# Kernel optimization log

Measured on AMD Instinct MI355X. Metric: run time of the kernel, lower is better.

## Reference

```python
import jax, jax.numpy as jnp
import numpy as np

N_NODES = 100000
N_EDGES = 800000
C = 64        # in_channels == out_channels
H = 4         # num_heads
LN_EPS = 1e-5
SM_EPS = 1e-8


def setup_inputs() -> dict:
    key = jax.random.key(0)
    ks = jax.random.split(key, 8)
    return {
        "x": jax.random.normal(ks[0], (N_NODES, C), dtype=jnp.float32),
        "edge_index": jax.random.randint(ks[1], (2, N_EDGES), 0, N_NODES, dtype=jnp.int64),
        "edge_time": jax.random.uniform(ks[2], (N_EDGES,), dtype=jnp.float32),
        "current_time": 1,
        "W_w": jax.random.normal(ks[3], (C, C), dtype=jnp.float32) * (1.0 / np.sqrt(C)),
        "W_b": jnp.zeros((C,), dtype=jnp.float32),
        "attn_w": jax.random.normal(ks[4], (2 * C, H), dtype=jnp.float32) * (1.0 / np.sqrt(2 * C)),
        "attn_b": jnp.zeros((H,), dtype=jnp.float32),
        "decay_rate": jnp.full((1,), 0.1, dtype=jnp.float32),
        "proj_w": jax.random.normal(ks[5], (C * H, C), dtype=jnp.float32) * (1.0 / np.sqrt(C * H)),
        "proj_b": jnp.zeros((C,), dtype=jnp.float32),
        "ln_g": jnp.ones((C,), dtype=jnp.float32),
        "ln_b": jnp.zeros((C,), dtype=jnp.float32),
    }


def reference(x, edge_index, edge_time, current_time, W_w, W_b, attn_w, attn_b,
              decay_rate, proj_w, proj_b, ln_g, ln_b):
    num_nodes = x.shape[0]
    src, dst = edge_index[0], edge_index[1]

    # relation-specific transform (same Linear applied to src and dst node sets)
    h = x @ W_w + W_b                       # (N, C)
    h_src = h[src]                          # (E, C) gather
    h_dst = h[dst]                          # (E, C) gather

    # attention: Linear(2C -> H) + LeakyReLU(0.2)
    logits = h_src @ attn_w[:C] + h_dst @ attn_w[C:] + attn_b   # (E, H)
    scores = jax.nn.leaky_relu(logits, negative_slope=0.2)

    # temporal decay: exp(-softplus(lambda) * delta_t), multiplied pre-softmax
    delta_t = jnp.float32(current_time) - edge_time             # (E,)
    lam = jax.nn.softplus(decay_rate[0])
    scores = scores * jnp.exp(-lam * delta_t)[:, None]

    # segmented (per-destination) softmax over incoming edges
    smax = jax.ops.segment_max(scores, dst, num_segments=num_nodes)   # (N, H)
    e = jnp.exp(scores - smax[dst])                                   # (E, H)
    ssum = jax.ops.segment_sum(e, dst, num_segments=num_nodes)        # (N, H)
    attn = e / (ssum[dst] + SM_EPS)                                   # (E, H)

    # per-edge messages (E, C, H) -> (E, C*H), scatter-add to destinations
    msg = (h_src[:, :, None] * attn[:, None, :]).reshape(-1, C * H)
    agg = jax.ops.segment_sum(msg, dst, num_segments=num_nodes)       # (N, C*H)

    # single edge type -> mean over 1 message is identity
    out = agg @ proj_w + proj_b                                       # (N, C)
    # dropout p=0 (eval) -> identity; residual + LayerNorm + ReLU
    z = out + x
    mu = jnp.mean(z, axis=-1, keepdims=True)
    var = jnp.mean(jnp.square(z - mu), axis=-1, keepdims=True)
    y = ln_g * (z - mu) * jax.lax.rsqrt(var + LN_EPS) + ln_b
    return jax.nn.relu(y)
```

## Files before the change

kernel.cpp:

```cpp
#include <hip/hip_runtime.h>


typedef __attribute__((ext_vector_type(8))) short bf16x8;
typedef __attribute__((ext_vector_type(4))) float f32x4;

__device__ __forceinline__ unsigned short f2bf(float f) {
  unsigned int u = __float_as_uint(f);
  u += 0x7FFFu + ((u >> 16) & 1u);
  return (unsigned short)(u >> 16);
}
__device__ __forceinline__ float bf2f(unsigned short s) {
  return __uint_as_float(((unsigned int)s) << 16);
}
__device__ __forceinline__ unsigned int pk(float a, float b) {
  return (unsigned int)f2bf(a) | ((unsigned int)f2bf(b) << 16);
}
__device__ __forceinline__ float bflo(int u) {
  return __uint_as_float(((unsigned int)u) << 16);
}
__device__ __forceinline__ float bfhi(int u) {
  return __uint_as_float(((unsigned int)u) & 0xFFFF0000u);
}

__device__ __forceinline__ void split8(float4 a, float4 b, bf16x8* hi, bf16x8* lo) {
  float f[8] = {a.x, a.y, a.z, a.w, b.x, b.y, b.z, b.w};
  bf16x8 h, l;
  #pragma unroll
  for (int j = 0; j < 8; ++j) {
    unsigned short hs = f2bf(f[j]);
    h[j] = (short)hs;
    l[j] = (short)f2bf(f[j] - bf2f(hs));
  }
  *hi = h; *lo = l;
}

__global__ __launch_bounds__(256) void k_init(const float* __restrict__ Pw,
    const float* __restrict__ Ww, const float* __restrict__ Wb,
    const float* __restrict__ aw, unsigned short* __restrict__ Bf,
    unsigned short* __restrict__ Ah, unsigned short* __restrict__ Al,
    float* __restrict__ bc, int* __restrict__ deg, int N, int NBn)
{
  if ((int)blockIdx.x == NBn) {
    int t = threadIdx.x;
    for (int i = t; i < 5120; i += 256) {
      int j = i & 7, lane = (i >> 3) & 63, ks = (i >> 9) & 1, rb = i >> 10;
      int row = rb * 16 + (lane & 15);
      int k   = ks * 32 + (lane >> 4) * 8 + j;
      float w = 0.f;
      if (row < 64) {
        w = Ww[(size_t)k * 64 + row];
      } else if (row < 72) {
        int jj = row - 64;
        const float* ac = (jj < 4) ? (aw + jj) : (aw + 256 + (jj - 4));
        float s = 0.f;
        for (int c = 0; c < 64; ++c) s = fmaf(Ww[(size_t)k * 64 + c], ac[c * 4], s);
        w = s;
      }
      unsigned short hh = f2bf(w);
      Ah[i] = hh;
      Al[i] = f2bf(w - bf2f(hh));
    }
    if (t < 80) {
      float b = 0.f;
      if (t < 64) {
        b = Wb[t];
      } else if (t < 72) {
        int jj = t - 64;
        const float* ac = (jj < 4) ? (aw + jj) : (aw + 256 + (jj - 4));
        float s = 0.f;
        for (int c = 0; c < 64; ++c) s = fmaf(Wb[c], ac[c * 4], s);
        b = s;
      }
      bc[t] = b;
    }
    return;
  }
  int i = blockIdx.x * 256 + threadIdx.x;
  if (i < N) deg[i] = 0;
  if (i < 16384) {
    int j    = i & 7;
    int lane = (i >> 3) & 63;
    int cb   = (i >> 9) & 3;
    int ks   = i >> 11;
    int k    = ks * 32 + (lane >> 4) * 8 + j;
    int colg = cb * 16 + (lane & 15);
    Bf[i] = f2bf(Pw[(size_t)k * 64 + colg]);
  }
}

#define RBSTEP(ACC, RB) { \
  bf16x8 fh0 = *(const bf16x8*)(Ah + ((RB * 2 + 0) * 64 + lane) * 8); \
  bf16x8 fl0 = *(const bf16x8*)(Al + ((RB * 2 + 0) * 64 + lane) * 8); \
  bf16x8 fh1 = *(const bf16x8*)(Ah + ((RB * 2 + 1) * 64 + lane) * 8); \
  bf16x8 fl1 = *(const bf16x8*)(Al + ((RB * 2 + 1) * 64 + lane) * 8); \
  ACC = __builtin_amdgcn_mfma_f32_16x16x32_bf16(fh0, bh0, ACC, 0, 0, 0); \
  ACC = __builtin_amdgcn_mfma_f32_16x16x32_bf16(fl0, bh0, ACC, 0, 0, 0); \
  ACC = __builtin_amdgcn_mfma_f32_16x16x32_bf16(fh0, bl0, ACC, 0, 0, 0); \
  ACC = __builtin_amdgcn_mfma_f32_16x16x32_bf16(fh1, bh1, ACC, 0, 0, 0); \
  ACC = __builtin_amdgcn_mfma_f32_16x16x32_bf16(fl1, bh1, ACC, 0, 0, 0); \
  ACC = __builtin_amdgcn_mfma_f32_16x16x32_bf16(fh1, bl1, ACC, 0, 0, 0); \
}

__global__ __launch_bounds__(256, 4) void k_hd(const float* __restrict__ x,
    const unsigned short* __restrict__ Ah, const unsigned short* __restrict__ Al,
    const float* __restrict__ bc, const int* __restrict__ ei,
    unsigned short* __restrict__ h16, float4* __restrict__ u,
    float4* __restrict__ v, int* __restrict__ deg, int* __restrict__ rank,
    int N, int E, int NBe)
{
  if ((int)blockIdx.x < NBe) {
    int e0 = blockIdx.x * 1024 + threadIdx.x * 4;
    if (e0 + 3 < E) {
      int4 d4 = *(const int4*)(ei + E + e0);
      int4 r4;
      r4.x = atomicAdd(&deg[d4.x], 1);
      r4.y = atomicAdd(&deg[d4.y], 1);
      r4.z = atomicAdd(&deg[d4.z], 1);
      r4.w = atomicAdd(&deg[d4.w], 1);
      *(int4*)(rank + e0) = r4;
    } else {
      for (int e = e0; e < E; ++e) rank[e] = atomicAdd(&deg[ei[E + e]], 1);
    }
    return;
  }
  const int lane = threadIdx.x & 63;
  const int wv   = threadIdx.x >> 6;
  const int col  = lane & 15;
  const int quad = lane >> 4;

  const float4 bc0 = *(const float4*)(bc +  0 + quad * 4);
  const float4 bc1 = *(const float4*)(bc + 16 + quad * 4);
  const float4 bc2 = *(const float4*)(bc + 32 + quad * 4);
  const float4 bc3 = *(const float4*)(bc + 48 + quad * 4);
  const float4 bc4 = *(const float4*)(bc + 64 + quad * 4);

  const int base0 = (blockIdx.x - NBe) * 256 + wv * 64;
  for (int st = 0; st < 4; ++st) {
    const int node = base0 + st * 16 + col;
    const bool val = (node < N);
    const int nc = val ? node : N - 1;
    const float* xr = x + (size_t)nc * 64 + quad * 8;
    float4 x0 = *(const float4*)(xr);
    float4 x1 = *(const float4*)(xr + 4);
    float4 x2 = *(const float4*)(xr + 32);
    float4 x3 = *(const float4*)(xr + 36);
    bf16x8 bh0, bl0, bh1, bl1;
    split8(x0, x1, &bh0, &bl0);
    split8(x2, x3, &bh1, &bl1);

    f32x4 a0 = {0.f, 0.f, 0.f, 0.f};
    f32x4 a1 = {0.f, 0.f, 0.f, 0.f};
    f32x4 a2 = {0.f, 0.f, 0.f, 0.f};
    f32x4 a3 = {0.f, 0.f, 0.f, 0.f};
    f32x4 a4 = {0.f, 0.f, 0.f, 0.f};
    RBSTEP(a0, 0);
    RBSTEP(a1, 1);
    RBSTEP(a2, 2);
    RBSTEP(a3, 3);
    RBSTEP(a4, 4);

    if (val) {
      unsigned short* hr = h16 + (size_t)node * 64 + quad * 4;
      uint2 w0, w1, w2, w3;
      w0.x = pk(a0[0] + bc0.x, a0[1] + bc0.y);
      w0.y = pk(a0[2] + bc0.z, a0[3] + bc0.w);
      w1.x = pk(a1[0] + bc1.x, a1[1] + bc1.y);
      w1.y = pk(a1[2] + bc1.z, a1[3] + bc1.w);
      w2.x = pk(a2[0] + bc2.x, a2[1] + bc2.y);
      w2.y = pk(a2[2] + bc2.z, a2[3] + bc2.w);
      w3.x = pk(a3[0] + bc3.x, a3[1] + bc3.y);
      w3.y = pk(a3[2] + bc3.z, a3[3] + bc3.w);
      *(uint2*)(hr)      = w0;
      *(uint2*)(hr + 16) = w1;
      *(uint2*)(hr + 32) = w2;
      *(uint2*)(hr + 48) = w3;
      if (quad == 0)
        u[node] = make_float4(a4[0] + bc4.x, a4[1] + bc4.y, a4[2] + bc4.z, a4[3] + bc4.w);
      else if (quad == 1)
        v[node] = make_float4(a4[0] + bc4.x, a4[1] + bc4.y, a4[2] + bc4.z, a4[3] + bc4.w);
    }
  }
}

__global__ __launch_bounds__(256) void scan1(const int* __restrict__ deg,
    int* __restrict__ offs, int* __restrict__ bsums, int N)
{
  int i = blockIdx.x * 256 + threadIdx.x;
  int lane = threadIdx.x & 63;
  int w = threadIdx.x >> 6;
  int v = (i < N) ? deg[i] : 0;
  int s = v;
  #pragma unroll
  for (int d = 1; d < 64; d <<= 1) {
    int t = __shfl_up(s, d, 64);
    if (lane >= d) s += t;
  }
  __shared__ int wsum[4];
  if (lane == 63) wsum[w] = s;
  __syncthreads();
  int add = 0;
  if (w > 0) add += wsum[0];
  if (w > 1) add += wsum[1];
  if (w > 2) add += wsum[2];
  if (i < N) offs[i] = s - v + add;
  if (threadIdx.x == 255) bsums[blockIdx.x] = wsum[0] + wsum[1] + wsum[2] + wsum[3];
}

__global__ __launch_bounds__(512) void scan2(int* bsums, int NB)
{
  __shared__ int lds[512];
  int t = threadIdx.x;
  int v = (t < NB) ? bsums[t] : 0;
  lds[t] = v;
  __syncthreads();
  for (int s = 1; s < 512; s <<= 1) {
    int a = (t >= s) ? lds[t - s] : 0;
    __syncthreads();
    lds[t] += a;
    __syncthreads();
  }
  if (t < NB) bsums[t] = lds[t] - v;
}

__global__ __launch_bounds__(256) void k_fill(const int* __restrict__ ei,
    const float* __restrict__ et, const int* __restrict__ ctime,
    const float* __restrict__ drate, const float4* __restrict__ u,
    const float4* __restrict__ v, const float* __restrict__ attn_b,
    const int* __restrict__ offs, const int* __restrict__ bsums,
    const int* __restrict__ rank, int4* __restrict__ csr, int E)
{
  int e = blockIdx.x * 256 + threadIdx.x;
  if (e >= E) return;
  const int s = ei[e];
  const int d = ei[E + e];
  const float4 us = u[s];
  const float4 vd = v[d];
  const float4 ab = *(const float4*)attn_b;
  const float lam = log1pf(__expf(drate[0]));
  const float w = __expf(-lam * ((float)ctime[0] - et[e]));

  float4 o; float t;
  t = us.x + vd.x + ab.x; t = (t > 0.f ? t : 0.2f * t) * w; o.x = __expf(t);
  t = us.y + vd.y + ab.y; t = (t > 0.f ? t : 0.2f * t) * w; o.y = __expf(t);
  t = us.z + vd.z + ab.z; t = (t > 0.f ? t : 0.2f * t) * w; o.z = __expf(t);
  t = us.w + vd.w + ab.w; t = (t > 0.f ? t : 0.2f * t) * w; o.w = __expf(t);

  int4 rec;
  rec.x = s;
  rec.y = (int)pk(o.x, o.y);
  rec.z = (int)pk(o.z, o.w);
  rec.w = 0;
  csr[offs[d] + bsums[d >> 8] + rank[e]] = rec;
}

__global__ __launch_bounds__(256) void k_agg(const unsigned short* __restrict__ h16,
    const int4* __restrict__ csr, const int* __restrict__ offs,
    const int* __restrict__ bsums, unsigned short* __restrict__ agg,
    int N, int E)
{
  const int c = threadIdx.x & 63;
  const int wid = blockIdx.x * 4 + (threadIdx.x >> 6);
  const int wstride = gridDim.x * 4;

  for (int n0 = wid; n0 < N; n0 += wstride) {
    const int n = __builtin_amdgcn_readfirstlane(n0);
    const int p0 = offs[n] + bsums[n >> 8];
    const int p1 = (n + 1 < N) ? (offs[n + 1] + bsums[(n + 1) >> 8]) : E;
    const int nf = (p1 - p0) & ~3;

    float acc0 = 0.f, acc1 = 0.f, acc2 = 0.f, acc3 = 0.f;
    float den0 = 0.f, den1 = 0.f, den2 = 0.f, den3 = 0.f;

    int4 rA0, rA1, rA2, rA3;
    float gA0 = 0.f, gA1 = 0.f, gA2 = 0.f, gA3 = 0.f;
    if (nf) {
      rA0 = csr[p0];     rA1 = csr[p0 + 1];
      rA2 = csr[p0 + 2]; rA3 = csr[p0 + 3];
      gA0 = bf2f(h16[(size_t)rA0.x * 64 + c]);
      gA1 = bf2f(h16[(size_t)rA1.x * 64 + c]);
      gA2 = bf2f(h16[(size_t)rA2.x * 64 + c]);
      gA3 = bf2f(h16[(size_t)rA3.x * 64 + c]);
    }
    for (int p = p0; p < p0 + nf; p += 4) {
      int4 rB0, rB1, rB2, rB3;
      float gB0, gB1, gB2, gB3;
      const bool more = (p + 4 < p0 + nf);
      if (more) {
        rB0 = csr[p + 4]; rB1 = csr[p + 5];
        rB2 = csr[p + 6]; rB3 = csr[p + 7];
        gB0 = bf2f(h16[(size_t)rB0.x * 64 + c]);
        gB1 = bf2f(h16[(size_t)rB1.x * 64 + c]);
        gB2 = bf2f(h16[(size_t)rB2.x * 64 + c]);
        gB3 = bf2f(h16[(size_t)rB3.x * 64 + c]);
      }
      float e00 = bflo(rA0.y), e01 = bfhi(rA0.y), e02 = bflo(rA0.z), e03 = bfhi(rA0.z);
      float e10 = bflo(rA1.y), e11 = bfhi(rA1.y), e12 = bflo(rA1.z), e13 = bfhi(rA1.z);
      float e20 = bflo(rA2.y), e21 = bfhi(rA2.y), e22 = bflo(rA2.z), e23 = bfhi(rA2.z);
      float e30 = bflo(rA3.y), e31 = bfhi(rA3.y), e32 = bflo(rA3.z), e33 = bfhi(rA3.z);
      den0 += (e00 + e10) + (e20 + e30);
      den1 += (e01 + e11) + (e21 + e31);
      den2 += (e02 + e12) + (e22 + e32);
      den3 += (e03 + e13) + (e23 + e33);
      acc0 = fmaf(e00, gA0, fmaf(e10, gA1, fmaf(e20, gA2, fmaf(e30, gA3, acc0))));
      acc1 = fmaf(e01, gA0, fmaf(e11, gA1, fmaf(e21, gA2, fmaf(e31, gA3, acc1))));
      acc2 = fmaf(e02, gA0, fmaf(e12, gA1, fmaf(e22, gA2, fmaf(e32, gA3, acc2))));
      acc3 = fmaf(e03, gA0, fmaf(e13, gA1, fmaf(e23, gA2, fmaf(e33, gA3, acc3))));
      if (more) {
        rA0 = rB0; rA1 = rB1; rA2 = rB2; rA3 = rB3;
        gA0 = gB0; gA1 = gB1; gA2 = gB2; gA3 = gB3;
      }
    }
    for (int p = p0 + nf; p < p1; ++p) {
      int4 r = csr[p];
      float g = bf2f(h16[(size_t)r.x * 64 + c]);
      float e0 = bflo(r.y), e1 = bfhi(r.y), e2 = bflo(r.z), e3 = bfhi(r.z);
      den0 += e0; den1 += e1; den2 += e2; den3 += e3;
      acc0 = fmaf(e0, g, acc0);
      acc1 = fmaf(e1, g, acc1);
      acc2 = fmaf(e2, g, acc2);
      acc3 = fmaf(e3, g, acc3);
    }
    uint2 w;
    w.x = pk(acc0 / (den0 + 1e-8f), acc1 / (den1 + 1e-8f));
    w.y = pk(acc2 / (den2 + 1e-8f), acc3 / (den3 + 1e-8f));
    *(uint2*)(agg + (size_t)n * 256 + c * 4) = w;
  }
}

__global__ __launch_bounds__(256) void k_projm(const unsigned short* __restrict__ agg,
    const unsigned short* __restrict__ Bf, const float* __restrict__ x,
    const float* __restrict__ Pb,
    const float* __restrict__ lg, const float* __restrict__ lb,
    float* __restrict__ out, int N)
{
  const int lane = threadIdx.x & 63;
  const int wv = threadIdx.x >> 6;
  const int nt = blockIdx.x * 4 + wv;
  if (nt * 16 >= N) return;
  const int col  = lane & 15;
  const int quad = lane >> 4;
  const int base = nt * 16;

  int na = base + col; if (na >= N) na = N - 1;
  const unsigned short* aptr = agg + (size_t)na * 256 + quad * 8;

  f32x4 acc0 = {0.f, 0.f, 0.f, 0.f};
  f32x4 acc1 = {0.f, 0.f, 0.f, 0.f};
  f32x4 acc2 = {0.f, 0.f, 0.f, 0.f};
  f32x4 acc3 = {0.f, 0.f, 0.f, 0.f};

  #pragma unroll
  for (int ks = 0; ks < 8; ++ks) {
    bf16x8 av = *(const bf16x8*)(aptr + ks * 32);
    bf16x8 b0 = *(const bf16x8*)(Bf + ((size_t)(ks * 4 + 0) * 64 + lane) * 8);
    bf16x8 b1 = *(const bf16x8*)(Bf + ((size_t)(ks * 4 + 1) * 64 + lane) * 8);
    bf16x8 b2 = *(const bf16x8*)(Bf + ((size_t)(ks * 4 + 2) * 64 + lane) * 8);
    bf16x8 b3 = *(const bf16x8*)(Bf + ((size_t)(ks * 4 + 3) * 64 + lane) * 8);
    acc0 = __builtin_amdgcn_mfma_f32_16x16x32_bf16(av, b0, acc0, 0, 0, 0);
    acc1 = __builtin_amdgcn_mfma_f32_16x16x32_bf16(av, b1, acc1, 0, 0, 0);
    acc2 = __builtin_amdgcn_mfma_f32_16x16x32_bf16(av, b2, acc2, 0, 0, 0);
    acc3 = __builtin_amdgcn_mfma_f32_16x16x32_bf16(av, b3, acc3, 0, 0, 0);
  }

  const float pb0 = Pb[col], pb1 = Pb[16 + col], pb2 = Pb[32 + col], pb3 = Pb[48 + col];
  float v[4][4];
  #pragma unroll
  for (int r = 0; r < 4; ++r) {
    int node = base + quad * 4 + r; if (node >= N) node = N - 1;
    const float* xr = x + (size_t)node * 64;
    v[0][r] = acc0[r] + pb0 + xr[col];
    v[1][r] = acc1[r] + pb1 + xr[16 + col];
    v[2][r] = acc2[r] + pb2 + xr[32 + col];
    v[3][r] = acc3[r] + pb3 + xr[48 + col];
  }

  float mu[4], inv[4];
  #pragma unroll
  for (int r = 0; r < 4; ++r) {
    float s = (v[0][r] + v[1][r]) + (v[2][r] + v[3][r]);
    s += __shfl_xor(s, 1, 64); s += __shfl_xor(s, 2, 64);
    s += __shfl_xor(s, 4, 64); s += __shfl_xor(s, 8, 64);
    mu[r] = s * 0.015625f;
  }
  #pragma unroll
  for (int r = 0; r < 4; ++r) {
    float d0 = v[0][r] - mu[r], d1 = v[1][r] - mu[r];
    float d2 = v[2][r] - mu[r], d3 = v[3][r] - mu[r];
    float s = fmaf(d0, d0, d1 * d1) + fmaf(d2, d2, d3 * d3);
    s += __shfl_xor(s, 1, 64); s += __shfl_xor(s, 2, 64);
    s += __shfl_xor(s, 4, 64); s += __shfl_xor(s, 8, 64);
    inv[r] = rsqrtf(s * 0.015625f + 1e-5f);
  }

  const float lg0 = lg[col], lg1 = lg[16 + col], lg2 = lg[32 + col], lg3 = lg[48 + col];
  const float lb0 = lb[col], lb1 = lb[16 + col], lb2 = lb[32 + col], lb3 = lb[48 + col];
  #pragma unroll
  for (int r = 0; r < 4; ++r) {
    int node = base + quad * 4 + r;
    if (node < N) {
      float* orow = out + (size_t)node * 64;
      orow[col]      = fmaxf(fmaf(lg0 * (v[0][r] - mu[r]), inv[r], lb0), 0.f);
      orow[16 + col] = fmaxf(fmaf(lg1 * (v[1][r] - mu[r]), inv[r], lb1), 0.f);
      orow[32 + col] = fmaxf(fmaf(lg2 * (v[2][r] - mu[r]), inv[r], lb2), 0.f);
      orow[48 + col] = fmaxf(fmaf(lg3 * (v[3][r] - mu[r]), inv[r], lb3), 0.f);
    }
  }
}

extern "C" void kernel_launch(void* const* d_in, const int* in_sizes, int n_in,
                              void* d_out, int out_size, void* d_ws, size_t ws_size,
                              hipStream_t stream)
{
  const float* x  = (const float*)d_in[0];
  const int*   ei = (const int*)d_in[1];
  const float* et = (const float*)d_in[2];
  const int*   ct = (const int*)d_in[3];
  const float* Ww = (const float*)d_in[4];
  const float* Wb = (const float*)d_in[5];
  const float* aw = (const float*)d_in[6];
  const float* ab = (const float*)d_in[7];
  const float* dr = (const float*)d_in[8];
  const float* Pw = (const float*)d_in[9];
  const float* Pb = (const float*)d_in[10];
  const float* lg = (const float*)d_in[11];
  const float* lb = (const float*)d_in[12];
  float* out = (float*)d_out;

  const int N = in_sizes[0] / 64;
  const int E = in_sizes[2];

  char* ws = (char*)d_ws;
  size_t off = 0;
  auto take = [&](size_t bytes) -> char* {
    char* p = ws + off;
    off = (off + bytes + 255) & ~(size_t)255;
    return p;
  };
  unsigned short* h16 = (unsigned short*)take((size_t)N * 64 * 2);
  int*    deg    = (int*)take((size_t)N * 4);
  int*    offs   = (int*)take((size_t)N * 4);
  int*    bsums  = (int*)take(512 * 4);
  int*    rank   = (int*)take((size_t)E * 4);
  int4*   csr    = (int4*)take((size_t)E * 16);
  unsigned short* agg = (unsigned short*)take((size_t)N * 256 * 2);
  float4* u      = (float4*)take((size_t)N * 16);
  float4* v      = (float4*)take((size_t)N * 16);
  unsigned short* Bf = (unsigned short*)take(16384 * 2);
  unsigned short* Ah = (unsigned short*)take(5120 * 2);
  unsigned short* Al = (unsigned short*)take(5120 * 2);
  float*  bc     = (float*)take(80 * 4);

  const int NBn  = (N + 255) / 256;
  const int NBe  = (E + 255) / 256;
  const int NBe4 = (E + 1023) / 1024;

  k_init<<<NBn + 1, 256, 0, stream>>>(Pw, Ww, Wb, aw, Bf, Ah, Al, bc, deg, N, NBn);
  k_hd<<<NBe4 + NBn, 256, 0, stream>>>(x, Ah, Al, bc, ei, h16, u, v, deg, rank, N, E, NBe4);
  scan1<<<NBn, 256, 0, stream>>>(deg, offs, bsums, N);
  scan2<<<1, 512, 0, stream>>>(bsums, NBn);
  k_fill<<<NBe, 256, 0, stream>>>(ei, et, ct, dr, u, v, ab, offs, bsums, rank, csr, E);
  k_agg<<<2048, 256, 0, stream>>>(h16, csr, offs, bsums, agg, N, E);
  const int NT = (N + 15) / 16;
  k_projm<<<(NT + 3) / 4, 256, 0, stream>>>(agg, Bf, x, Pb, lg, lb, out, N);
}
```

Before: 266.2 us.

## Replace per-node atomic CSR build with binned counting sort and LDS-sorted aggregation

```diff
diff --git a/kernel.cpp b/kernel.cpp
--- a/kernel.cpp
+++ b/kernel.cpp
@@ -3,6 +3,12 @@
 
 typedef __attribute__((ext_vector_type(8))) short bf16x8;
 typedef __attribute__((ext_vector_type(4))) float f32x4;
+
+#define CHUNK  2048
+#define BINSH  5
+#define BINSZ  32
+#define MAXBIN 3200
+#define MAXREC 1024
 
 __device__ __forceinline__ unsigned short f2bf(float f) {
   unsigned int u = __float_as_uint(f);
@@ -36,11 +42,25 @@
 
 __global__ __launch_bounds__(256) void k_init(const float* __restrict__ Pw,
     const float* __restrict__ Ww, const float* __restrict__ Wb,
-    const float* __restrict__ aw, unsigned short* __restrict__ Bf,
-    unsigned short* __restrict__ Ah, unsigned short* __restrict__ Al,
-    float* __restrict__ bc, int* __restrict__ deg, int N, int NBn)
-{
-  if ((int)blockIdx.x == NBn) {
+    const float* __restrict__ aw, const int* __restrict__ ei,
+    unsigned short* __restrict__ Bf, unsigned short* __restrict__ Ah,
+    unsigned short* __restrict__ Al, float* __restrict__ bc,
+    int* __restrict__ histM, int E, int NBIN)
+{
+  __shared__ int hist[MAXBIN];
+  const int b = blockIdx.x;
+  if (b < 64) {
+    int i = b * 256 + threadIdx.x;
+    int j    = i & 7;
+    int lane = (i >> 3) & 63;
+    int cb   = (i >> 9) & 3;
+    int ks   = i >> 11;
+    int k    = ks * 32 + (lane >> 4) * 8 + j;
+    int colg = cb * 16 + (lane & 15);
+    Bf[i] = f2bf(Pw[(size_t)k * 64 + colg]);
+    return;
+  }
+  if (b == 64) {
     int t = threadIdx.x;
     for (int i = t; i < 5120; i += 256) {
       int j = i & 7, lane = (i >> 3) & 63, ks = (i >> 9) & 1, rb = i >> 10;
@@ -61,31 +81,42 @@
       Al[i] = f2bf(w - bf2f(hh));
     }
     if (t < 80) {
-      float b = 0.f;
+      float bb = 0.f;
       if (t < 64) {
-        b = Wb[t];
+        bb = Wb[t];
       } else if (t < 72) {
         int jj = t - 64;
         const float* ac = (jj < 4) ? (aw + jj) : (aw + 256 + (jj - 4));
         float s = 0.f;
         for (int c = 0; c < 64; ++c) s = fmaf(Wb[c], ac[c * 4], s);
-        b = s;
+        bb = s;
       }
-      bc[t] = b;
+      bc[t] = bb;
     }
     return;
   }
-  int i = blockIdx.x * 256 + threadIdx.x;
-  if (i < N) deg[i] = 0;
-  if (i < 16384) {
-    int j    = i & 7;
-    int lane = (i >> 3) & 63;
-    int cb   = (i >> 9) & 3;
-    int ks   = i >> 11;
-    int k    = ks * 32 + (lane >> 4) * 8 + j;
-    int colg = cb * 16 + (lane & 15);
-    Bf[i] = f2bf(Pw[(size_t)k * 64 + colg]);
-  }
+  const int cb = b - 65;
+  for (int i = threadIdx.x; i < NBIN; i += 256) hist[i] = 0;
+  __syncthreads();
+  const int base = cb * CHUNK + threadIdx.x * 8;
+  const int* dptr = ei + E;
+  if (base + 7 < E) {
+    int4 d0 = *(const int4*)(dptr + base);
+    int4 d1 = *(const int4*)(dptr + base + 4);
+    atomicAdd(&hist[d0.x >> BINSH], 1);
+    atomicAdd(&hist[d0.y >> BINSH], 1);
+    atomicAdd(&hist[d0.z >> BINSH], 1);
+    atomicAdd(&hist[d0.w >> BINSH], 1);
+    atomicAdd(&hist[d1.x >> BINSH], 1);
+    atomicAdd(&hist[d1.y >> BINSH], 1);
+    atomicAdd(&hist[d1.z >> BINSH], 1);
+    atomicAdd(&hist[d1.w >> BINSH], 1);
+  } else {
+    for (int e = base; e < E; ++e) atomicAdd(&hist[dptr[e] >> BINSH], 1);
+  }
+  __syncthreads();
+  for (int i = threadIdx.x; i < NBIN; i += 256)
+    histM[(size_t)cb * NBIN + i] = hist[i];
 }
 
 #define RBSTEP(ACC, RB) { \
@@ -103,26 +134,9 @@
 
 __global__ __launch_bounds__(256, 4) void k_hd(const float* __restrict__ x,
     const unsigned short* __restrict__ Ah, const unsigned short* __restrict__ Al,
-    const float* __restrict__ bc, const int* __restrict__ ei,
-    unsigned short* __restrict__ h16, float4* __restrict__ u,
-    float4* __restrict__ v, int* __restrict__ deg, int* __restrict__ rank,
-    int N, int E, int NBe)
-{
-  if ((int)blockIdx.x < NBe) {
-    int e0 = blockIdx.x * 1024 + threadIdx.x * 4;
-    if (e0 + 3 < E) {
-      int4 d4 = *(const int4*)(ei + E + e0);
-      int4 r4;
-      r4.x = atomicAdd(&deg[d4.x], 1);
-      r4.y = atomicAdd(&deg[d4.y], 1);
-      r4.z = atomicAdd(&deg[d4.z], 1);
-      r4.w = atomicAdd(&deg[d4.w], 1);
-      *(int4*)(rank + e0) = r4;
-    } else {
-      for (int e = e0; e < E; ++e) rank[e] = atomicAdd(&deg[ei[E + e]], 1);
-    }
-    return;
-  }
+    const float* __restrict__ bc, unsigned short* __restrict__ h16,
+    float4* __restrict__ u, float4* __restrict__ v, int N)
+{
   const int lane = threadIdx.x & 63;
   const int wv   = threadIdx.x >> 6;
   const int col  = lane & 15;
@@ -134,7 +148,7 @@
   const float4 bc3 = *(const float4*)(bc + 48 + quad * 4);
   const float4 bc4 = *(const float4*)(bc + 64 + quad * 4);
 
-  const int base0 = (blockIdx.x - NBe) * 256 + wv * 64;
+  const int base0 = blockIdx.x * 256 + wv * 64;
   for (int st = 0; st < 4; ++st) {
     const int node = base0 + st * 16 + col;
     const bool val = (node < N);
@@ -182,6 +196,21 @@
   }
 }
 
+__global__ __launch_bounds__(256) void k_colscan(int* __restrict__ histM,
+    int* __restrict__ bintot, int NBIN, int NCH)
+{
+  const int bin = blockIdx.x * 256 + threadIdx.x;
+  if (bin >= NBIN) return;
+  int run = 0;
+  for (int b = 0; b < NCH; ++b) {
+    size_t idx = (size_t)b * NBIN + bin;
+    int v = histM[idx];
+    histM[idx] = run;
+    run += v;
+  }
+  bintot[bin] = run;
+}
+
 __global__ __launch_bounds__(256) void scan1(const int* __restrict__ deg,
     int* __restrict__ offs, int* __restrict__ bsums, int N)
 {
@@ -222,103 +251,132 @@
   if (t < NB) bsums[t] = lds[t] - v;
 }
 
-__global__ __launch_bounds__(256) void k_fill(const int* __restrict__ ei,
+__global__ __launch_bounds__(256) void k_fill2(const int* __restrict__ ei,
     const float* __restrict__ et, const int* __restrict__ ctime,
     const float* __restrict__ drate, const float4* __restrict__ u,
     const float4* __restrict__ v, const float* __restrict__ attn_b,
-    const int* __restrict__ offs, const int* __restrict__ bsums,
-    const int* __restrict__ rank, int4* __restrict__ csr, int E)
-{
-  int e = blockIdx.x * 256 + threadIdx.x;
-  if (e >= E) return;
-  const int s = ei[e];
-  const int d = ei[E + e];
-  const float4 us = u[s];
-  const float4 vd = v[d];
+    const int* __restrict__ offsb, const int* __restrict__ bsumsb,
+    const int* __restrict__ histM, int4* __restrict__ csr, int E, int NBIN)
+{
+  __shared__ int cur[MAXBIN];
+  const int cb = blockIdx.x;
+  for (int i = threadIdx.x; i < NBIN; i += 256)
+    cur[i] = offsb[i] + bsumsb[i >> 8] + histM[(size_t)cb * NBIN + i];
+  __syncthreads();
+
   const float4 ab = *(const float4*)attn_b;
   const float lam = log1pf(__expf(drate[0]));
-  const float w = __expf(-lam * ((float)ctime[0] - et[e]));
-
-  float4 o; float t;
-  t = us.x + vd.x + ab.x; t = (t > 0.f ? t : 0.2f * t) * w; o.x = __expf(t);
-  t = us.y + vd.y + ab.y; t = (t > 0.f ? t : 0.2f * t) * w; o.y = __expf(t);
-  t = us.z + vd.z + ab.z; t = (t > 0.f ? t : 0.2f * t) * w; o.z = __expf(t);
-  t = us.w + vd.w + ab.w; t = (t > 0.f ? t : 0.2f * t) * w; o.w = __expf(t);
-
-  int4 rec;
-  rec.x = s;
-  rec.y = (int)pk(o.x, o.y);
-  rec.z = (int)pk(o.z, o.w);
-  rec.w = 0;
-  csr[offs[d] + bsums[d >> 8] + rank[e]] = rec;
-}
-
-__global__ __launch_bounds__(256) void k_agg(const unsigned short* __restrict__ h16,
-    const int4* __restrict__ csr, const int* __restrict__ offs,
-    const int* __restrict__ bsums, unsigned short* __restrict__ agg,
-    int N, int E)
-{
-  const int c = threadIdx.x & 63;
-  const int wid = blockIdx.x * 4 + (threadIdx.x >> 6);
-  const int wstride = gridDim.x * 4;
-
-  for (int n0 = wid; n0 < N; n0 += wstride) {
-    const int n = __builtin_amdgcn_readfirstlane(n0);
-    const int p0 = offs[n] + bsums[n >> 8];
-    const int p1 = (n + 1 < N) ? (offs[n + 1] + bsums[(n + 1) >> 8]) : E;
-    const int nf = (p1 - p0) & ~3;
+  const float ctf = (float)ctime[0];
+  const int base = cb * CHUNK + threadIdx.x * 8;
+
+  auto doedge = [&](int s, int d, float tv) {
+    const float4 us = u[s];
+    const float4 vd = v[d];
+    const float w = __expf(-lam * (ctf - tv));
+    float4 o; float t;
+    t = us.x + vd.x + ab.x; t = (t > 0.f ? t : 0.2f * t) * w; o.x = __expf(t);
+    t = us.y + vd.y + ab.y; t = (t > 0.f ? t : 0.2f * t) * w; o.y = __expf(t);
+    t = us.z + vd.z + ab.z; t = (t > 0.f ? t : 0.2f * t) * w; o.z = __expf(t);
+    t = us.w + vd.w + ab.w; t = (t > 0.f ? t : 0.2f * t) * w; o.w = __expf(t);
+    int slot = atomicAdd(&cur[d >> BINSH], 1);
+    int4 rec;
+    rec.x = s;
+    rec.y = (int)pk(o.x, o.y);
+    rec.z = (int)pk(o.z, o.w);
+    rec.w = d & (BINSZ - 1);
+    csr[slot] = rec;
+  };
+
+  if (base + 7 < E) {
+    int4 s0 = *(const int4*)(ei + base);
+    int4 s1 = *(const int4*)(ei + base + 4);
+    int4 d0 = *(const int4*)(ei + E + base);
+    int4 d1 = *(const int4*)(ei + E + base + 4);
+    float4 t0 = *(const float4*)(et + base);
+    float4 t1 = *(const float4*)(et + base + 4);
+    doedge(s0.x, d0.x, t0.x);
+    doedge(s0.y, d0.y, t0.y);
+    doedge(s0.z, d0.z, t0.z);
+    doedge(s0.w, d0.w, t0.w);
+    doedge(s1.x, d1.x, t1.x);
+    doedge(s1.y, d1.y, t1.y);
+    doedge(s1.z, d1.z, t1.z);
+    doedge(s1.w, d1.w, t1.w);
+  } else {
+    for (int e = base; e < E; ++e) doedge(ei[e], ei[E + e], et[e]);
+  }
+}
+
+__global__ __launch_bounds__(256) void k_aggb(const unsigned short* __restrict__ h16,
+    const int4* __restrict__ csr, const int* __restrict__ offsb,
+    const int* __restrict__ bsumsb, unsigned short* __restrict__ agg,
+    int N, int E, int NBIN)
+{
+  __shared__ int4 srec[MAXREC];
+  __shared__ int hcnt[BINSZ];
+  __shared__ int nbase[BINSZ + 1];
+  __shared__ int cur[BINSZ];
+
+  const int bin = blockIdx.x;
+  const int start = offsb[bin] + bsumsb[bin >> 8];
+  const int end0  = (bin + 1 < NBIN) ? (offsb[bin + 1] + bsumsb[(bin + 1) >> 8]) : E;
+  const int cnt = min(end0 - start, MAXREC);
+
+  if (threadIdx.x < BINSZ) hcnt[threadIdx.x] = 0;
+  __syncthreads();
+
+  int4 r0 = {0,0,0,0}, r1 = {0,0,0,0}, r2 = {0,0,0,0}, r3 = {0,0,0,0};
+  const int i0 = threadIdx.x, i1 = i0 + 256, i2 = i0 + 512, i3 = i0 + 768;
+  const bool b0 = i0 < cnt, b1 = i1 < cnt, b2 = i2 < cnt, b3 = i3 < cnt;
+  if (b0) { r0 = csr[start + i0]; atomicAdd(&hcnt[r0.w], 1); }
+  if (b1) { r1 = csr[start + i1]; atomicAdd(&hcnt[r1.w], 1); }
+  if (b2) { r2 = csr[start + i2]; atomicAdd(&hcnt[r2.w], 1); }
+  if (b3) { r3 = csr[start + i3]; atomicAdd(&hcnt[r3.w], 1); }
+  __syncthreads();
+  if (threadIdx.x == 0) {
+    int run = 0;
+    #pragma unroll
+    for (int i = 0; i < BINSZ; ++i) { nbase[i] = run; cur[i] = run; run += hcnt[i]; }
+    nbase[BINSZ] = run;
+  }
+  __syncthreads();
+  if (b0) srec[atomicAdd(&cur[r0.w], 1)] = r0;
+  if (b1) srec[atomicAdd(&cur[r1.w], 1)] = r1;
+  if (b2) srec[atomicAdd(&cur[r2.w], 1)] = r2;
+  if (b3) srec[atomicAdd(&cur[r3.w], 1)] = r3;
+  __syncthreads();
+
+  const int c  = threadIdx.x & 63;
+  const int wv = threadIdx.x >> 6;
+  for (int nl = wv; nl < BINSZ; nl += 4) {
+    const int n = bin * BINSZ + nl;
+    if (n >= N) break;
+    const int p0 = nbase[nl], p1 = nbase[nl + 1];
 
     float acc0 = 0.f, acc1 = 0.f, acc2 = 0.f, acc3 = 0.f;
     float den0 = 0.f, den1 = 0.f, den2 = 0.f, den3 = 0.f;
 
-    int4 rA0, rA1, rA2, rA3;
-    float gA0 = 0.f, gA1 = 0.f, gA2 = 0.f, gA3 = 0.f;
-    if (nf) {
-      rA0 = csr[p0];     rA1 = csr[p0 + 1];
-      rA2 = csr[p0 + 2]; rA3 = csr[p0 + 3];
-      gA0 = bf2f(h16[(size_t)rA0.x * 64 + c]);
-      gA1 = bf2f(h16[(size_t)rA1.x * 64 + c]);
-      gA2 = bf2f(h16[(size_t)rA2.x * 64 + c]);
-      gA3 = bf2f(h16[(size_t)rA3.x * 64 + c]);
+    int p = p0;
+    int4 rA = {0,0,0,0};
+    float gA = 0.f;
+    if (p < p1) {
+      rA = srec[p];
+      gA = bf2f(h16[(size_t)rA.x * 64 + c]);
     }
-    for (int p = p0; p < p0 + nf; p += 4) {
-      int4 rB0, rB1, rB2, rB3;
-      float gB0, gB1, gB2, gB3;
-      const bool more = (p + 4 < p0 + nf);
+    for (; p < p1; ++p) {
+      int4 rB; float gB = 0.f;
+      const bool more = (p + 1 < p1);
       if (more) {
-        rB0 = csr[p + 4]; rB1 = csr[p + 5];
-        rB2 = csr[p + 6]; rB3 = csr[p + 7];
-        gB0 = bf2f(h16[(size_t)rB0.x * 64 + c]);
-        gB1 = bf2f(h16[(size_t)rB1.x * 64 + c]);
-        gB2 = bf2f(h16[(size_t)rB2.x * 64 + c]);
-        gB3 = bf2f(h16[(size_t)rB3.x * 64 + c]);
+        rB = srec[p + 1];
+        gB = bf2f(h16[(size_t)rB.x * 64 + c]);
       }
-      float e00 = bflo(rA0.y), e01 = bfhi(rA0.y), e02 = bflo(rA0.z), e03 = bfhi(rA0.z);
-      float e10 = bflo(rA1.y), e11 = bfhi(rA1.y), e12 = bflo(rA1.z), e13 = bfhi(rA1.z);
-      float e20 = bflo(rA2.y), e21 = bfhi(rA2.y), e22 = bflo(rA2.z), e23 = bfhi(rA2.z);
-      float e30 = bflo(rA3.y), e31 = bfhi(rA3.y), e32 = bflo(rA3.z), e33 = bfhi(rA3.z);
-      den0 += (e00 + e10) + (e20 + e30);
-      den1 += (e01 + e11) + (e21 + e31);
-      den2 += (e02 + e12) + (e22 + e32);
-      den3 += (e03 + e13) + (e23 + e33);
-      acc0 = fmaf(e00, gA0, fmaf(e10, gA1, fmaf(e20, gA2, fmaf(e30, gA3, acc0))));
-      acc1 = fmaf(e01, gA0, fmaf(e11, gA1, fmaf(e21, gA2, fmaf(e31, gA3, acc1))));
-      acc2 = fmaf(e02, gA0, fmaf(e12, gA1, fmaf(e22, gA2, fmaf(e32, gA3, acc2))));
-      acc3 = fmaf(e03, gA0, fmaf(e13, gA1, fmaf(e23, gA2, fmaf(e33, gA3, acc3))));
-      if (more) {
-        rA0 = rB0; rA1 = rB1; rA2 = rB2; rA3 = rB3;
-        gA0 = gB0; gA1 = gB1; gA2 = gB2; gA3 = gB3;
-      }
-    }
-    for (int p = p0 + nf; p < p1; ++p) {
-      int4 r = csr[p];
-      float g = bf2f(h16[(size_t)r.x * 64 + c]);
-      float e0 = bflo(r.y), e1 = bfhi(r.y), e2 = bflo(r.z), e3 = bfhi(r.z);
+      float e0 = bflo(rA.y), e1 = bfhi(rA.y), e2 = bflo(rA.z), e3 = bfhi(rA.z);
       den0 += e0; den1 += e1; den2 += e2; den3 += e3;
-      acc0 = fmaf(e0, g, acc0);
-      acc1 = fmaf(e1, g, acc1);
-      acc2 = fmaf(e2, g, acc2);
-      acc3 = fmaf(e3, g, acc3);
+      acc0 = fmaf(e0, gA, acc0);
+      acc1 = fmaf(e1, gA, acc1);
+      acc2 = fmaf(e2, gA, acc2);
+      acc3 = fmaf(e3, gA, acc3);
+      if (more) { rA = rB; gA = gB; }
     }
     uint2 w;
     w.x = pk(acc0 / (den0 + 1e-8f), acc1 / (den1 + 1e-8f));
@@ -428,6 +486,9 @@
 
   const int N = in_sizes[0] / 64;
   const int E = in_sizes[2];
+  const int NBIN = (N + BINSZ - 1) >> BINSH;
+  const int NCH  = (E + CHUNK - 1) / CHUNK;
+  const int NB2  = (NBIN + 255) / 256;
 
   char* ws = (char*)d_ws;
   size_t off = 0;
@@ -437,10 +498,6 @@
     return p;
   };
   unsigned short* h16 = (unsigned short*)take((size_t)N * 64 * 2);
-  int*    deg    = (int*)take((size_t)N * 4);
-  int*    offs   = (int*)take((size_t)N * 4);
-  int*    bsums  = (int*)take(512 * 4);
-  int*    rank   = (int*)take((size_t)E * 4);
   int4*   csr    = (int4*)take((size_t)E * 16);
   unsigned short* agg = (unsigned short*)take((size_t)N * 256 * 2);
   float4* u      = (float4*)take((size_t)N * 16);
@@ -449,17 +506,20 @@
   unsigned short* Ah = (unsigned short*)take(5120 * 2);
   unsigned short* Al = (unsigned short*)take(5120 * 2);
   float*  bc     = (float*)take(80 * 4);
-
-  const int NBn  = (N + 255) / 256;
-  const int NBe  = (E + 255) / 256;
-  const int NBe4 = (E + 1023) / 1024;
-
-  k_init<<<NBn + 1, 256, 0, stream>>>(Pw, Ww, Wb, aw, Bf, Ah, Al, bc, deg, N, NBn);
-  k_hd<<<NBe4 + NBn, 256, 0, stream>>>(x, Ah, Al, bc, ei, h16, u, v, deg, rank, N, E, NBe4);
-  scan1<<<NBn, 256, 0, stream>>>(deg, offs, bsums, N);
-  scan2<<<1, 512, 0, stream>>>(bsums, NBn);
-  k_fill<<<NBe, 256, 0, stream>>>(ei, et, ct, dr, u, v, ab, offs, bsums, rank, csr, E);
-  k_agg<<<2048, 256, 0, stream>>>(h16, csr, offs, bsums, agg, N, E);
+  int*    histM  = (int*)take((size_t)NCH * NBIN * 4);
+  int*    bintot = (int*)take((size_t)NBIN * 4);
+  int*    offsb  = (int*)take((size_t)NBIN * 4);
+  int*    bsumsb = (int*)take(512 * 4);
+
+  const int NBn = (N + 255) / 256;
+
+  k_init<<<65 + NCH, 256, 0, stream>>>(Pw, Ww, Wb, aw, ei, Bf, Ah, Al, bc, histM, E, NBIN);
+  k_hd<<<NBn, 256, 0, stream>>>(x, Ah, Al, bc, h16, u, v, N);
+  k_colscan<<<NB2, 256, 0, stream>>>(histM, bintot, NBIN, NCH);
+  scan1<<<NB2, 256, 0, stream>>>(bintot, offsb, bsumsb, NBIN);
+  scan2<<<1, 512, 0, stream>>>(bsumsb, NB2);
+  k_fill2<<<NCH, 256, 0, stream>>>(ei, et, ct, dr, u, v, ab, offsb, bsumsb, histM, csr, E, NBIN);
+  k_aggb<<<NBIN, 256, 0, stream>>>(h16, csr, offsb, bsumsb, agg, N, E, NBIN);
   const int NT = (N + 15) / 16;
   k_projm<<<(NT + 3) / 4, 256, 0, stream>>>(agg, Bf, x, Pb, lg, lb, out, N);
 }
```

Result: slower. 373.8 us (+40.4%).
